# Kernel optimization log

Hardware: AMD Instinct MI355X
Metric: run time of the kernel (lower is better)

Reference implementation:

```python
import jax, jax.numpy as jnp
import numpy as np

TAPS_INT = [-12, -34, -56, -42, 18, 120, 260, 380, 400, 290, 60, -210, -430, -500,
            -380, -120, 180, 430, 540, 480, 280, 20, -220, -370, -400, -310, -150,
            10, 120, 160, 130, 60]
SCALE = 65536  # power-of-two fixed-point scale -> floor(acc/SCALE) is exact in fp32
L = len(TAPS_INT)  # 32 taps
N = 16777216       # 2^24 samples


def setup_inputs() -> dict:
    key = jax.random.key(0)
    # integer-valued samples; |x| < ~1000 keeps all intermediate sums exactly
    # representable in float32 (< 2^24), so this matches the int64 torch math.
    x = jnp.round(jax.random.normal(key, (N,), dtype=jnp.float32) * 170.0)
    taps = jnp.asarray(TAPS_INT, dtype=jnp.float32)
    return {"x": x, "taps": taps}


def reference(x, taps):
    n_len = x.shape[0]
    xi = jnp.trunc(x)  # x.to(torch.int64) truncates toward zero (no-op here: x integral)
    # causal FIR: acc[n] = sum_k x[n-k] * taps[k]  == full convolution, first N samples
    acc = jnp.convolve(xi, taps, mode='full')[:n_len]
    y = jnp.floor(acc / SCALE)  # acc // scale (floor division), exact: SCALE = 2^16
    n = jnp.arange(n_len)
    # original loop runs for n in [L, N); y[0:L] stays zero
    return jnp.where(n >= L, y, 0.0).astype(jnp.float32)
```

## Files before the change

kernel.cpp:

```cpp
#include <hip/hip_runtime.h>
#include <math.h>

__device__ __constant__ const float TAPS[32] = {
    -12.f,  -34.f,  -56.f,  -42.f,   18.f,  120.f,  260.f,  380.f,
    400.f,  290.f,   60.f, -210.f, -430.f, -500.f, -380.f, -120.f,
    180.f,  430.f,  540.f,  480.f,  280.f,   20.f, -220.f, -370.f,
   -400.f, -310.f, -150.f,   10.f,  120.f,  160.f,  130.f,   60.f
};

#define SCALE_INV (1.0f / 65536.0f)
#define NT_BLOCKS 2048
#define NT_THREADS 256

typedef float floatx4 __attribute__((ext_vector_type(4)));

__global__ __launch_bounds__(NT_THREADS)
void fir32_persist(const float* __restrict__ x, float* __restrict__ y, int n) {
    const long nchunks = (long)n >> 3;
    const long stride = (long)NT_BLOCKS * NT_THREADS;
    const long gtid = (long)blockIdx.x * NT_THREADS + threadIdx.x;

    const floatx4* x4 = reinterpret_cast<const floatx4*>(x);
    floatx4* y4 = reinterpret_cast<floatx4*>(y);

    for (long c = gtid; c < nchunks; c += stride) {
        const long o4 = 2L * c;
        const bool head = (c < 4);

        float w[40];
        #pragma unroll
        for (int q = 0; q < 10; ++q) {
            long i4 = o4 - 8 + q;
            i4 = (i4 < 0) ? 0 : i4;
            floatx4 v = x4[i4];
            w[4 * q + 0] = v.x;
            w[4 * q + 1] = v.y;
            w[4 * q + 2] = v.z;
            w[4 * q + 3] = v.w;
        }

        float acc[8];
        #pragma unroll
        for (int j = 0; j < 8; ++j) {
            float a = 0.0f;
            #pragma unroll
            for (int k = 0; k < 32; ++k) {
                a = fmaf(w[32 + j - k], TAPS[k], a);
            }
            acc[j] = head ? 0.0f : floorf(a * SCALE_INV);
        }

        floatx4 out0 = { acc[0], acc[1], acc[2], acc[3] };
        floatx4 out1 = { acc[4], acc[5], acc[6], acc[7] };
        __builtin_nontemporal_store(out0, &y4[o4]);
        __builtin_nontemporal_store(out1, &y4[o4 + 1]);
    }
}

extern "C" void kernel_launch(void* const* d_in, const int* in_sizes, int n_in,
                              void* d_out, int out_size, void* d_ws, size_t ws_size,
                              hipStream_t stream) {
    const float* x = (const float*)d_in[0];
    float* y = (float*)d_out;
    const int n = in_sizes[0];

    fir32_persist<<<dim3(NT_BLOCKS), dim3(NT_THREADS), 0, stream>>>(x, y, n);
}
```

Before: 27.51 us.

## Software-pipeline FIR loop with double-buffered register windows

```diff
diff --git a/kernel.cpp b/kernel.cpp
--- a/kernel.cpp
+++ b/kernel.cpp
@@ -1,7 +1,7 @@
 #include <hip/hip_runtime.h>
 #include <math.h>
 
-__device__ __constant__ const float TAPS[32] = {
+__device__ __constant__ float TAPS[32] = {
     -12.f,  -34.f,  -56.f,  -42.f,   18.f,  120.f,  260.f,  380.f,
     400.f,  290.f,   60.f, -210.f, -430.f, -500.f, -380.f, -120.f,
     180.f,  430.f,  540.f,  480.f,  280.f,   20.f, -220.f, -370.f,
@@ -9,51 +9,69 @@
 };
 
 #define SCALE_INV (1.0f / 65536.0f)
-#define NT_BLOCKS 2048
-#define NT_THREADS 256
+#define NB  2048
+#define NTH 256
 
 typedef float floatx4 __attribute__((ext_vector_type(4)));
 
-__global__ __launch_bounds__(NT_THREADS)
-void fir32_persist(const float* __restrict__ x, float* __restrict__ y, int n) {
+__device__ __forceinline__ void load_win(const floatx4* __restrict__ x4,
+                                         long c, floatx4 v[10], bool clamp) {
+    const long o4 = 2 * c;
+    #pragma unroll
+    for (int q = 0; q < 10; ++q) {
+        long i4 = o4 - 8 + q;
+        if (clamp) i4 = (i4 < 0) ? 0 : i4;
+        v[q] = x4[i4];
+    }
+}
+
+__device__ __forceinline__ void comp_store(const floatx4 v[10], long c,
+                                           floatx4* __restrict__ y4) {
+    const bool head = (c < 4);
+    float acc[8];
+    #pragma unroll
+    for (int j = 0; j < 8; ++j) {
+        float a = 0.0f;
+        #pragma unroll
+        for (int k = 0; k < 32; ++k) {
+            const int m = 32 + j - k;
+            a = fmaf(v[m >> 2][m & 3], TAPS[k], a);
+        }
+        acc[j] = head ? 0.0f : floorf(a * SCALE_INV);
+    }
+    floatx4 o0 = {acc[0], acc[1], acc[2], acc[3]};
+    floatx4 o1 = {acc[4], acc[5], acc[6], acc[7]};
+    __builtin_nontemporal_store(o0, &y4[2 * c]);
+    __builtin_nontemporal_store(o1, &y4[2 * c + 1]);
+}
+
+__global__ __launch_bounds__(NTH)
+void fir32_pipe(const float* __restrict__ x, float* __restrict__ y, int n) {
     const long nchunks = (long)n >> 3;
-    const long stride = (long)NT_BLOCKS * NT_THREADS;
-    const long gtid = (long)blockIdx.x * NT_THREADS + threadIdx.x;
+    const long stride = (long)NB * NTH;
+    long c = (long)blockIdx.x * NTH + threadIdx.x;
+    if (c >= nchunks) return;
 
     const floatx4* x4 = reinterpret_cast<const floatx4*>(x);
     floatx4* y4 = reinterpret_cast<floatx4*>(y);
 
-    for (long c = gtid; c < nchunks; c += stride) {
-        const long o4 = 2L * c;
-        const bool head = (c < 4);
+    floatx4 A[10], B[10];
+    load_win(x4, c, A, true);
+    while (true) {
+        const long c2 = c + stride;
+        const bool has2 = (c2 < nchunks);
+        if (has2) load_win(x4, c2, B, false);
+        __builtin_amdgcn_sched_barrier(0);
+        comp_store(A, c, y4);
+        if (!has2) return;
 
-        float w[40];
-        #pragma unroll
-        for (int q = 0; q < 10; ++q) {
-            long i4 = o4 - 8 + q;
-            i4 = (i4 < 0) ? 0 : i4;
-            floatx4 v = x4[i4];
-            w[4 * q + 0] = v.x;
-            w[4 * q + 1] = v.y;
-            w[4 * q + 2] = v.z;
-            w[4 * q + 3] = v.w;
-        }
-
-        float acc[8];
-        #pragma unroll
-        for (int j = 0; j < 8; ++j) {
-            float a = 0.0f;
-            #pragma unroll
-            for (int k = 0; k < 32; ++k) {
-                a = fmaf(w[32 + j - k], TAPS[k], a);
-            }
-            acc[j] = head ? 0.0f : floorf(a * SCALE_INV);
-        }
-
-        floatx4 out0 = { acc[0], acc[1], acc[2], acc[3] };
-        floatx4 out1 = { acc[4], acc[5], acc[6], acc[7] };
-        __builtin_nontemporal_store(out0, &y4[o4]);
-        __builtin_nontemporal_store(out1, &y4[o4 + 1]);
+        const long c3 = c2 + stride;
+        const bool has3 = (c3 < nchunks);
+        if (has3) load_win(x4, c3, A, false);
+        __builtin_amdgcn_sched_barrier(0);
+        comp_store(B, c2, y4);
+        if (!has3) return;
+        c = c3;
     }
 }
 
@@ -64,5 +82,5 @@
     float* y = (float*)d_out;
     const int n = in_sizes[0];
 
-    fir32_persist<<<dim3(NT_BLOCKS), dim3(NT_THREADS), 0, stream>>>(x, y, n);
+    fir32_pipe<<<dim3(NB), dim3(NTH), 0, stream>>>(x, y, n);
 }
```

After: 29.45 us. 1.07x slower.
